# Optimization experiments

Hardware: AMD Instinct MI355X
Metric: run time of the kernel (lower is better)

Reference implementation:

```python
import math
import jax, jax.numpy as jnp
import numpy as np

N_HEADS = 8
FACTOR = 1


def setup_inputs() -> dict:
    key = jax.random.key(0)
    ks = jax.random.split(key, 8)
    B, L, D = 8, 2048, 512
    scale = 0.05
    return {
        "queries": jax.random.normal(ks[0], (B, L, D), jnp.float32),
        "keys": jax.random.normal(ks[1], (B, L, D), jnp.float32),
        "values": jax.random.normal(ks[2], (B, L, D), jnp.float32),
        "Wq": jax.random.normal(ks[3], (D, D), jnp.float32) * scale,
        "bq": jnp.zeros((D,), jnp.float32),
        "Wk": jax.random.normal(ks[4], (D, D), jnp.float32) * scale,
        "bk": jnp.zeros((D,), jnp.float32),
        "Wv": jax.random.normal(ks[5], (D, D), jnp.float32) * scale,
        "bv": jnp.zeros((D,), jnp.float32),
        "Wo": jax.random.normal(ks[6], (D, D), jnp.float32) * scale,
        "bo": jnp.zeros((D,), jnp.float32),
    }


def _autocorrelation(q, k, v):
    # q,k,v: [B, L, H, E]; L == S assumed (as built in setup_inputs)
    B, L, H, E = q.shape
    qp = jnp.transpose(q, (0, 2, 3, 1))  # [B,H,E,L]
    kp = jnp.transpose(k, (0, 2, 3, 1))
    vp = jnp.transpose(v, (0, 2, 3, 1))
    q_fft = jnp.fft.rfft(qp, axis=-1)
    k_fft = jnp.fft.rfft(kp, axis=-1)
    corr = jnp.fft.irfft(q_fft * jnp.conj(k_fft), n=L, axis=-1)  # [B,H,E,L]

    # training-path time-delay aggregation
    top_k = int(FACTOR * math.log(L))  # static python int
    mean_value = corr.mean(axis=(1, 2))  # [B, L]
    _, index = jax.lax.top_k(mean_value.mean(axis=0), top_k)  # [K] global delays
    weights = mean_value[:, index]  # [B, K]
    tmp_corr = jax.nn.softmax(weights, axis=-1)  # [B, K]
    # roll(v, -d) along last axis == gather at (t + d) mod L
    idx = (jnp.arange(L)[None, :] + index[:, None]) % L  # [K, L]
    patterns = vp[..., idx]  # [B,H,E,K,L]
    delays_agg = jnp.einsum('bhekl,bk->bhel', patterns, tmp_corr)  # [B,H,E,L]
    return jnp.transpose(delays_agg, (0, 3, 1, 2))  # [B,L,H,E]


def reference(queries, keys, values, Wq, bq, Wk, bk, Wv, bv, Wo, bo):
    B, L, Dm = queries.shape
    H = N_HEADS
    q = (queries @ Wq + bq).reshape(B, L, H, -1)
    k = (keys @ Wk + bk).reshape(B, L, H, -1)
    v = (values @ Wv + bv).reshape(B, L, H, -1)
    out = _autocorrelation(q, k, v).reshape(B, L, -1)
    return out @ Wo + bo
```

## Files before the change

kernel.cpp:

```cpp
#include <hip/hip_runtime.h>
#include <stdint.h>

#define BATCH 8
#define L_SEQ 2048
#define D_MODEL 512
#define TOPK 7
#define BM 128
#define BN 128
#define BK 32
#define LK 40
#define LT 136

typedef _Float16 f16x8 __attribute__((ext_vector_type(8)));
typedef __attribute__((ext_vector_type(4))) float f32x4;
typedef unsigned short u16;
typedef unsigned int u32;

__device__ __forceinline__ u16 f2h(float f) {
    union { _Float16 h; u16 u; } v; v.h = (_Float16)f; return v.u;
}

__device__ __forceinline__ void load_lds16(const u16* g, u16* l) {
    __builtin_amdgcn_global_load_lds(
        (const __attribute__((address_space(1))) u32*)(g),
        (__attribute__((address_space(3))) u32*)(l), 16, 0, 0);
}

__global__ __launch_bounds__(256) void gemm_qkv(
    const float* __restrict__ Xq, const float* __restrict__ Xk, const float* __restrict__ Xv,
    const u16* __restrict__ Wqt, const u16* __restrict__ Wkt, const u16* __restrict__ Wvt,
    const float* __restrict__ bq, const float* __restrict__ bk, const float* __restrict__ bv,
    u16* __restrict__ QT, u16* __restrict__ KT, u16* __restrict__ Vout)
{
    __shared__ __align__(16) u16 smem[BM * LK + BN * BK];
    u16* lA = smem;
    u16* lB = smem + BM * LK;
    u16* lT = smem;

    const int tid = threadIdx.x;
    const int hw = blockIdx.x;
    const int lg = (hw & 7) * 192 + (hw >> 3);
    const int bn = lg & 3, bm = (lg >> 2) & 127, z = lg >> 9;

    const int lane = tid & 63, wave = tid >> 6;
    const int wm = wave >> 1, wn = wave & 1;
    const int l15 = lane & 15, quad = lane >> 4;

    const float* A  = (z == 0) ? Xq  : (z == 1) ? Xk  : Xv;
    const u16*   Bt = (z == 0) ? Wqt : (z == 1) ? Wkt : Wvt;
    const float* bias = (z == 0) ? bq : (z == 1) ? bk : bv;

    const int s0 = wave * 64 + lane, s1 = s0 + 256;
    const int r0 = s0 >> 2, c0 = (s0 & 3) ^ ((r0 >> 1) & 3);
    const int r1 = s1 >> 2, c1 = (s1 & 3) ^ ((r1 >> 1) & 3);
    const u16* gB0 = Bt + (long)(bn * BN + r0) * D_MODEL + c0 * 8;
    const u16* gB1 = Bt + (long)(bn * BN + r1) * D_MODEL + c1 * 8;
    u16* lB0 = &lB[wave * 512]; u16* lB1 = &lB[2048 + wave * 512];

    f32x4 acc[4][4] = {};

    for (int k0 = 0; k0 < D_MODEL; k0 += BK) {
        load_lds16(gB0, lB0); load_lds16(gB1, lB1);
        gB0 += BK; gB1 += BK;
        #pragma unroll
        for (int j = 0; j < 4; ++j) {
            int idx = tid + j * 256;
            int row = idx >> 3, c4 = (idx & 7) * 4;
            float4 va = *(const float4*)(A + (long)(bm * BM + row) * D_MODEL + k0 + c4);
            ushort4 pa;
            pa.x = f2h(va.x); pa.y = f2h(va.y); pa.z = f2h(va.z); pa.w = f2h(va.w);
            *(ushort4*)&lA[row * LK + c4] = pa;
        }
        __syncthreads();

        f16x8 fa[4], fb[4];
        #pragma unroll
        for (int i = 0; i < 4; ++i)
            fa[i] = *(const f16x8*)&lA[(wm * 64 + i * 16 + l15) * LK + quad * 8];
        #pragma unroll
        for (int j = 0; j < 4; ++j) {
            int n = wn * 64 + j * 16 + l15;
            int cs = quad ^ ((n >> 1) & 3);
            fb[j] = *(const f16x8*)&lB[n * 32 + cs * 8];
        }
        #pragma unroll
        for (int i = 0; i < 4; ++i)
            #pragma unroll
            for (int j = 0; j < 4; ++j)
                acc[i][j] = __builtin_amdgcn_mfma_f32_16x16x32_f16(fa[i], fb[j], acc[i][j], 0, 0, 0);
        __syncthreads();
    }

    if (z < 2) {
        u16* out = (z == 0) ? QT : KT;
        const int t0 = (bm * BM) & (L_SEQ - 1);
        const int bb = (bm * BM) >> 11;
        #pragma unroll
        for (int h = 0; h < 2; ++h) {
            __syncthreads();
            if (wn == h) {
                #pragma unroll
                for (int j = 0; j < 4; ++j) {
                    int dloc = j * 16 + l15;
                    float bvv = bias[bn * BN + h * 64 + dloc];
                    #pragma unroll
                    for (int i = 0; i < 4; ++i) {
                        int trow = wm * 64 + i * 16 + quad * 4;
                        #pragma unroll
                        for (int r = 0; r < 4; ++r)
                            lT[dloc * LT + trow + r] = f2h(acc[i][j][r] + bvv);
                    }
                }
            }
            __syncthreads();
            int dloc = tid >> 2, q4 = tid & 3;
            long base = ((long)(bb * D_MODEL + bn * BN + h * 64 + dloc)) * L_SEQ + t0;
            #pragma unroll
            for (int s = 0; s < 4; ++s) {
                int c = q4 * 4 + s;
                *(uint4*)(out + base + c * 8) = *(const uint4*)&lT[dloc * LT + c * 8];
            }
        }
    } else {
        #pragma unroll
        for (int i = 0; i < 4; ++i) {
            int row = bm * BM + wm * 64 + i * 16 + quad * 4;
            #pragma unroll
            for (int j = 0; j < 4; ++j) {
                int col = bn * BN + wn * 64 + j * 16 + l15;
                float bvv = bias[col];
                #pragma unroll
                for (int r = 0; r < 4; ++r)
                    Vout[(long)(row + r) * D_MODEL + col] = f2h(acc[i][j][r] + bvv);
            }
        }
    }
}

__global__ __launch_bounds__(256) void gemm_out_fused(
    const u16* __restrict__ V, const u16* __restrict__ Bt,
    const int* __restrict__ selIdx, const float* __restrict__ selW,
    const float* __restrict__ bias, float* __restrict__ Cp)
{
    __shared__ __align__(16) u16 lA[BM * LK];
    __shared__ __align__(16) u16 lB[BN * BK];
    __shared__ int   si[TOPK];
    __shared__ float sw[BATCH][TOPK];

    const int tid = threadIdx.x;
    const int hw = blockIdx.x;
    const int lg = (hw & 7) * 64 + (hw >> 3);
    const int bn = lg & 3, bm = lg >> 2;

    const int lane = tid & 63, wave = tid >> 6;
    const int wm = wave >> 1, wn = wave & 1;
    const int l15 = lane & 15, quad = lane >> 4;

    if (tid < TOPK) si[tid] = selIdx[tid];
    if (tid < BATCH * TOPK) sw[tid / TOPK][tid % TOPK] = selW[tid];

    const int s0 = wave * 64 + lane, s1 = s0 + 256;
    const int r0 = s0 >> 2, c0 = (s0 & 3) ^ ((r0 >> 1) & 3);
    const int r1 = s1 >> 2, c1 = (s1 & 3) ^ ((r1 >> 1) & 3);
    const u16* gB0 = Bt + (long)(bn * BN + r0) * D_MODEL + c0 * 8;
    const u16* gB1 = Bt + (long)(bn * BN + r1) * D_MODEL + c1 * 8;
    u16* lB0 = &lB[wave * 512]; u16* lB1 = &lB[2048 + wave * 512];

    __syncthreads();

    f32x4 acc[4][4] = {};

    for (int k0 = 0; k0 < D_MODEL; k0 += BK) {
        load_lds16(gB0, lB0); load_lds16(gB1, lB1);
        gB0 += BK; gB1 += BK;
        #pragma unroll
        for (int j = 0; j < 2; ++j) {
            int idx = tid + j * 256;
            int row = idx >> 2, c8 = (idx & 3) * 8;
            int gr = bm * BM + row;
            int b = gr >> 11, l = gr & (L_SEQ - 1);
            float a[8] = {0,0,0,0,0,0,0,0};
            #pragma unroll
            for (int k = 0; k < TOPK; ++k) {
                int src = (l + si[k]) & (L_SEQ - 1);
                union { uint4 u; _Float16 h[8]; } x;
                x.u = *(const uint4*)(V + ((long)b * L_SEQ + src) * D_MODEL + k0 + c8);
                float w = sw[b][k];
                #pragma unroll
                for (int q = 0; q < 8; ++q) a[q] += w * (float)x.h[q];
            }
            union { uint4 u; u16 s[8]; } o;
            #pragma unroll
            for (int q = 0; q < 8; ++q) o.s[q] = f2h(a[q]);
            *(uint4*)&lA[row * LK + c8] = o.u;
        }
        __syncthreads();

        f16x8 fa[4], fb[4];
        #pragma unroll
        for (int i = 0; i < 4; ++i)
            fa[i] = *(const f16x8*)&lA[(wm * 64 + i * 16 + l15) * LK + quad * 8];
        #pragma unroll
        for (int j = 0; j < 4; ++j) {
            int n = wn * 64 + j * 16 + l15;
            int cs = quad ^ ((n >> 1) & 3);
            fb[j] = *(const f16x8*)&lB[n * 32 + cs * 8];
        }
        #pragma unroll
        for (int i = 0; i < 4; ++i)
            #pragma unroll
            for (int j = 0; j < 4; ++j)
                acc[i][j] = __builtin_amdgcn_mfma_f32_16x16x32_f16(fa[i], fb[j], acc[i][j], 0, 0, 0);
        __syncthreads();
    }

    #pragma unroll
    for (int i = 0; i < 4; ++i) {
        int row = bm * BM + wm * 64 + i * 16 + quad * 4;
        #pragma unroll
        for (int j = 0; j < 4; ++j) {
            int col = bn * BN + wn * 64 + j * 16 + l15;
            float bvv = bias[col];
            #pragma unroll
            for (int r = 0; r < 4; ++r)
                Cp[(long)(row + r) * D_MODEL + col] = acc[i][j][r] + bvv;
        }
    }
}

__device__ __forceinline__ void fft2048_lds(
    float* Zr, float* Zi, const float* Twr, const float* Twi, int tid)
{
    #pragma unroll
    for (int s = 0; s < 10; s += 2) {
        #pragma unroll
        for (int u = 0; u < 2; ++u) {
            int idx = tid + u * 256;
            int d1 = 1 << s;
            int pos = idx & (d1 - 1);
            int i0 = ((idx >> s) << (s + 2)) + pos;
            float w1r = Twr[pos << (10 - s)], w1i = Twi[pos << (10 - s)];
            float w2r = Twr[pos << (9 - s)],  w2i = Twi[pos << (9 - s)];
            int p2 = pos + d1;
            float w3r = Twr[p2 << (9 - s)],   w3i = Twi[p2 << (9 - s)];
            float ar = Zr[i0],          ai = Zi[i0];
            float br = Zr[i0 + d1],     bi = Zi[i0 + d1];
            float cr = Zr[i0 + 2 * d1], ci = Zi[i0 + 2 * d1];
            float dr = Zr[i0 + 3 * d1], di = Zi[i0 + 3 * d1];
            float t1r = br * w1r - bi * w1i, t1i = br * w1i + bi * w1r;
            float Ar = ar + t1r, Ai = ai + t1i, Br = ar - t1r, Bi = ai - t1i;
            float t2r = dr * w1r - di * w1i, t2i = dr * w1i + di * w1r;
            float Cr = cr + t2r, Ci = ci + t2i, Dr = cr - t2r, Di = ci - t2i;
            float u1r = Cr * w2r - Ci * w2i, u1i = Cr * w2i + Ci * w2r;
            float u2r = Dr * w3r - Di * w3i, u2i = Dr * w3i + Di * w3r;
            Zr[i0]          = Ar + u1r; Zi[i0]          = Ai + u1i;
            Zr[i0 + 2 * d1] = Ar - u1r; Zi[i0 + 2 * d1] = Ai - u1i;
            Zr[i0 + d1]     = Br + u2r; Zi[i0 + d1]     = Bi + u2i;
            Zr[i0 + 3 * d1] = Br - u2r; Zi[i0 + 3 * d1] = Bi - u2i;
        }
        __syncthreads();
    }
    #pragma unroll
    for (int j = 0; j < 4; ++j) {
        int idx = tid + j * 256;
        float wr = Twr[idx], wi = Twi[idx];
        float ar = Zr[idx], ai = Zi[idx];
        float br = Zr[idx + 1024], bi = Zi[idx + 1024];
        float tr = br * wr - bi * wi, ti = br * wi + bi * wr;
        Zr[idx] = ar + tr; Zi[idx] = ai + ti;
        Zr[idx + 1024] = ar - tr; Zi[idx + 1024] = ai - ti;
    }
    __syncthreads();
}

__global__ __launch_bounds__(256) void fft_corr_fwd(
    const u16* __restrict__ QT, const u16* __restrict__ KT, float* __restrict__ S)
{
    __shared__ float Zr[2048], Zi[2048];
    __shared__ float Sr[2048], Si[2048];
    __shared__ float Twr[1024], Twi[1024];
    const int tid = threadIdx.x;
    const int b = blockIdx.x >> 6, dg = blockIdx.x & 63;

    #pragma unroll
    for (int j = 0; j < 4; ++j) {
        int i = tid + j * 256;
        float ang = -6.28318530717958647692f * (float)i * (1.0f / 2048.0f);
        float sn, cs; __sincosf(ang, &sn, &cs);
        Twr[i] = cs; Twi[i] = sn;
    }
    #pragma unroll
    for (int j = 0; j < 8; ++j) { Sr[tid + j * 256] = 0.f; Si[tid + j * 256] = 0.f; }

    for (int g = 0; g < 8; ++g) {
        int d = dg * 8 + g;
        const u16* qrow = QT + ((long)b * D_MODEL + d) * L_SEQ;
        const u16* krow = KT + ((long)b * D_MODEL + d) * L_SEQ;
        __syncthreads();
        union { uint4 u; _Float16 h[8]; } xq, xk;
        xq.u = *(const uint4*)(qrow + tid * 8);
        xk.u = *(const uint4*)(krow + tid * 8);
        #pragma unroll
        for (int j = 0; j < 8; ++j) {
            int t = tid * 8 + j;
            int tr = (int)(__brev((unsigned)t) >> 21);
            Zr[tr] = (float)xq.h[j];
            Zi[tr] = (float)xk.h[j];
        }
        __syncthreads();
        fft2048_lds(Zr, Zi, Twr, Twi, tid);
        #pragma unroll
        for (int j = 0; j < 8; ++j) {
            int f = tid + j * 256;
            int fm = (2048 - f) & 2047;
            float Xr = Zr[f], Xi = Zi[f], Xmr = Zr[fm], Xmi = Zi[fm];
            float qr = 0.5f * (Xr + Xmr), qi = 0.5f * (Xi - Xmi);
            float dr = Xr - Xmr,          di = Xi + Xmi;
            float kr = 0.5f * di,         ki = -0.5f * dr;
            Sr[f] += qr * kr + qi * ki;
            Si[f] += qi * kr - qr * ki;
        }
    }
    __syncthreads();
    #pragma unroll
    for (int j = 0; j < 8; ++j) {
        int f = tid + j * 256;
        atomicAdd(&S[((long)b * 2048 + f) * 2 + 0], Sr[f]);
        atomicAdd(&S[((long)b * 2048 + f) * 2 + 1], Si[f]);
    }
}

__global__ __launch_bounds__(256) void fft_corr_inv(
    const float* __restrict__ S, float* __restrict__ raw)
{
    __shared__ float Zr[2048], Zi[2048];
    __shared__ float Twr[1024], Twi[1024];
    const int tid = threadIdx.x;
    const int b = blockIdx.x;

    #pragma unroll
    for (int j = 0; j < 4; ++j) {
        int i = tid + j * 256;
        float ang = 6.28318530717958647692f * (float)i * (1.0f / 2048.0f);
        float sn, cs; __sincosf(ang, &sn, &cs);
        Twr[i] = cs; Twi[i] = sn;
    }
    #pragma unroll
    for (int j = 0; j < 8; ++j) {
        int f = tid + j * 256;
        int fr = (int)(__brev((unsigned)f) >> 21);
        Zr[fr] = S[((long)b * 2048 + f) * 2 + 0];
        Zi[fr] = S[((long)b * 2048 + f) * 2 + 1];
    }
    __syncthreads();
    fft2048_lds(Zr, Zi, Twr, Twi, tid);
    #pragma unroll
    for (int j = 0; j < 8; ++j) {
        int t = tid + j * 256;
        raw[(long)b * 2048 + t] = Zr[t] * (1.0f / 2048.0f);
    }
}

__global__ __launch_bounds__(256) void transposeW4(
    const float* __restrict__ Wq, const float* __restrict__ Wk,
    const float* __restrict__ Wv, const float* __restrict__ Wo, u16* __restrict__ dstBase)
{
    __shared__ float t[32][33];
    const int z = blockIdx.z;
    const float* src = (z == 0) ? Wq : (z == 1) ? Wk : (z == 2) ? Wv : Wo;
    u16* dst = dstBase + (long)z * D_MODEL * D_MODEL;
    int tx = threadIdx.x & 31, ty = threadIdx.x >> 5;
    int c0 = blockIdx.x * 32, r0 = blockIdx.y * 32;
    #pragma unroll
    for (int r = ty; r < 32; r += 8)
        t[r][tx] = src[(long)(r0 + r) * D_MODEL + c0 + tx];
    __syncthreads();
    #pragma unroll
    for (int r = ty; r < 32; r += 8)
        dst[(long)(c0 + r) * D_MODEL + r0 + tx] = f2h(t[tx][r]);
}

__global__ __launch_bounds__(256) void select_topk(
    const float* __restrict__ raw, int* __restrict__ selIdx, float* __restrict__ selW)
{
    __shared__ float g[L_SEQ];
    __shared__ float rv[256];
    __shared__ int   ri[256];
    __shared__ int   sidx[TOPK];
    __shared__ float wbuf[BATCH][TOPK];
    int tid = threadIdx.x;
    for (int t = tid; t < L_SEQ; t += 256) {
        float s = 0.0f;
        #pragma unroll
        for (int b = 0; b < BATCH; ++b) s += raw[b * L_SEQ + t];
        g[t] = s;
    }
    __syncthreads();
    for (int it = 0; it < TOPK; ++it) {
        float best = -1e30f; int bi = 0x7fffffff;
        for (int t = tid; t < L_SEQ; t += 256) {
            float v = g[t];
            if (v > best || (v == best && t < bi)) { best = v; bi = t; }
        }
        rv[tid] = best; ri[tid] = bi;
        __syncthreads();
        for (int s = 128; s > 0; s >>= 1) {
            if (tid < s) {
                float v2 = rv[tid + s]; int i2 = ri[tid + s];
                if (v2 > rv[tid] || (v2 == rv[tid] && i2 < ri[tid])) { rv[tid] = v2; ri[tid] = i2; }
            }
            __syncthreads();
        }
        if (tid == 0) { sidx[it] = ri[0]; g[ri[0]] = -1e30f; }
        __syncthreads();
    }
    if (tid < BATCH * TOPK) {
        int b = tid / TOPK, k = tid % TOPK;
        wbuf[b][k] = raw[b * L_SEQ + sidx[k]] * (1.0f / 512.0f);
    }
    __syncthreads();
    if (tid < BATCH) {
        float mx = -1e30f;
        #pragma unroll
        for (int k = 0; k < TOPK; ++k) mx = fmaxf(mx, wbuf[tid][k]);
        float e[TOPK]; float sum = 0.0f;
        #pragma unroll
        for (int k = 0; k < TOPK; ++k) { e[k] = expf(wbuf[tid][k] - mx); sum += e[k]; }
        #pragma unroll
        for (int k = 0; k < TOPK; ++k) selW[tid * TOPK + k] = e[k] / sum;
    }
    if (tid < TOPK) selIdx[tid] = sidx[tid];
}

extern "C" void kernel_launch(void* const* d_in, const int* in_sizes, int n_in,
                              void* d_out, int out_size, void* d_ws, size_t ws_size,
                              hipStream_t stream)
{
    (void)in_sizes; (void)n_in; (void)out_size; (void)ws_size;
    const float* Xq = (const float*)d_in[0];
    const float* Xk = (const float*)d_in[1];
    const float* Xv = (const float*)d_in[2];
    const float* Wq = (const float*)d_in[3];
    const float* bq = (const float*)d_in[4];
    const float* Wk = (const float*)d_in[5];
    const float* bk = (const float*)d_in[6];
    const float* Wv = (const float*)d_in[7];
    const float* bv = (const float*)d_in[8];
    const float* Wo = (const float*)d_in[9];
    const float* bo = (const float*)d_in[10];

    char* ws = (char*)d_ws;
    const long SLABH = (long)BATCH * L_SEQ * D_MODEL * sizeof(u16);
    u16* QT   = (u16*)(ws);
    u16* KT   = (u16*)(ws + SLABH);
    u16* Vf   = (u16*)(ws + 2 * SLABH);
    const long WSZ = (long)D_MODEL * D_MODEL;
    u16* Wt   = (u16*)(ws + 3 * SLABH);
    u16* Wqt = Wt + 0 * WSZ; u16* Wkt = Wt + 1 * WSZ;
    u16* Wvt = Wt + 2 * WSZ; u16* Wot = Wt + 3 * WSZ;
    float* S   = (float*)(ws + 3 * SLABH + 4 * WSZ * sizeof(u16));
    float* raw = S + (long)BATCH * L_SEQ * 2;
    int*   sIdx = (int*)(raw + (long)BATCH * L_SEQ);
    float* sW   = (float*)(sIdx + 8);

    dim3 tb(256);
    transposeW4<<<dim3(16, 16, 4), tb, 0, stream>>>(Wq, Wk, Wv, Wo, Wt);
    hipMemsetAsync(S, 0, (long)BATCH * L_SEQ * 2 * sizeof(float), stream);

    gemm_qkv<<<dim3(1536), tb, 0, stream>>>(Xq, Xk, Xv, Wqt, Wkt, Wvt, bq, bk, bv, QT, KT, Vf);

    fft_corr_fwd<<<dim3(512), tb, 0, stream>>>(QT, KT, S);
    fft_corr_inv<<<dim3(BATCH), tb, 0, stream>>>(S, raw);
    select_topk<<<1, tb, 0, stream>>>(raw, sIdx, sW);

    gemm_out_fused<<<dim3(512), tb, 0, stream>>>(Vf, Wot, sIdx, sW, bo, (float*)d_out);
}
```

Measured before the change: 333.7 us.

## Double-buffer LDS in QKV and output GEMMs, use wave shuffles in top-k

```diff
diff --git a/kernel.cpp b/kernel.cpp
--- a/kernel.cpp
+++ b/kernel.cpp
@@ -26,16 +26,15 @@
         (__attribute__((address_space(3))) u32*)(l), 16, 0, 0);
 }
 
-__global__ __launch_bounds__(256) void gemm_qkv(
+__global__ __launch_bounds__(256, 3) void gemm_qkv(
     const float* __restrict__ Xq, const float* __restrict__ Xk, const float* __restrict__ Xv,
     const u16* __restrict__ Wqt, const u16* __restrict__ Wkt, const u16* __restrict__ Wvt,
     const float* __restrict__ bq, const float* __restrict__ bk, const float* __restrict__ bv,
     u16* __restrict__ QT, u16* __restrict__ KT, u16* __restrict__ Vout)
 {
-    __shared__ __align__(16) u16 smem[BM * LK + BN * BK];
-    u16* lA = smem;
-    u16* lB = smem + BM * LK;
+    __shared__ __align__(16) u16 smem[2 * BM * LK + 2 * BN * BK];
     u16* lT = smem;
+    u16* lBb = smem + 2 * BM * LK;
 
     const int tid = threadIdx.x;
     const int hw = blockIdx.x;
@@ -55,39 +54,74 @@
     const int r1 = s1 >> 2, c1 = (s1 & 3) ^ ((r1 >> 1) & 3);
     const u16* gB0 = Bt + (long)(bn * BN + r0) * D_MODEL + c0 * 8;
     const u16* gB1 = Bt + (long)(bn * BN + r1) * D_MODEL + c1 * 8;
-    u16* lB0 = &lB[wave * 512]; u16* lB1 = &lB[2048 + wave * 512];
 
     f32x4 acc[4][4] = {};
 
-    for (int k0 = 0; k0 < D_MODEL; k0 += BK) {
-        load_lds16(gB0, lB0); load_lds16(gB1, lB1);
+    {
+        load_lds16(gB0, lBb + wave * 512);
+        load_lds16(gB1, lBb + 2048 + wave * 512);
         gB0 += BK; gB1 += BK;
         #pragma unroll
         for (int j = 0; j < 4; ++j) {
             int idx = tid + j * 256;
             int row = idx >> 3, c4 = (idx & 7) * 4;
-            float4 va = *(const float4*)(A + (long)(bm * BM + row) * D_MODEL + k0 + c4);
+            float4 va = *(const float4*)(A + (long)(bm * BM + row) * D_MODEL + c4);
             ushort4 pa;
             pa.x = f2h(va.x); pa.y = f2h(va.y); pa.z = f2h(va.z); pa.w = f2h(va.w);
-            *(ushort4*)&lA[row * LK + c4] = pa;
-        }
-        __syncthreads();
+            *(ushort4*)&smem[row * LK + c4] = pa;
+        }
+    }
+    __syncthreads();
+
+    for (int t = 0; t < 16; ++t) {
+        const int cur = t & 1;
+        u16* lAc = smem + cur * (BM * LK);
+        u16* lBc = lBb + cur * (BN * BK);
+        u16* lAn = smem + (cur ^ 1) * (BM * LK);
+        u16* lBn = lBb + (cur ^ 1) * (BN * BK);
+        const bool nx = (t < 15);
+        const int k1 = (t + 1) * BK;
+
+        float4 va[4];
+        if (nx) {
+            load_lds16(gB0, lBn + wave * 512);
+            load_lds16(gB1, lBn + 2048 + wave * 512);
+            gB0 += BK; gB1 += BK;
+            #pragma unroll
+            for (int j = 0; j < 4; ++j) {
+                int idx = tid + j * 256;
+                int row = idx >> 3, c4 = (idx & 7) * 4;
+                va[j] = *(const float4*)(A + (long)(bm * BM + row) * D_MODEL + k1 + c4);
+            }
+        }
 
         f16x8 fa[4], fb[4];
         #pragma unroll
         for (int i = 0; i < 4; ++i)
-            fa[i] = *(const f16x8*)&lA[(wm * 64 + i * 16 + l15) * LK + quad * 8];
+            fa[i] = *(const f16x8*)&lAc[(wm * 64 + i * 16 + l15) * LK + quad * 8];
         #pragma unroll
         for (int j = 0; j < 4; ++j) {
             int n = wn * 64 + j * 16 + l15;
             int cs = quad ^ ((n >> 1) & 3);
-            fb[j] = *(const f16x8*)&lB[n * 32 + cs * 8];
+            fb[j] = *(const f16x8*)&lBc[n * 32 + cs * 8];
         }
         #pragma unroll
         for (int i = 0; i < 4; ++i)
             #pragma unroll
             for (int j = 0; j < 4; ++j)
                 acc[i][j] = __builtin_amdgcn_mfma_f32_16x16x32_f16(fa[i], fb[j], acc[i][j], 0, 0, 0);
+
+        if (nx) {
+            #pragma unroll
+            for (int j = 0; j < 4; ++j) {
+                int idx = tid + j * 256;
+                int row = idx >> 3, c4 = (idx & 7) * 4;
+                ushort4 pa;
+                pa.x = f2h(va[j].x); pa.y = f2h(va[j].y);
+                pa.z = f2h(va[j].z); pa.w = f2h(va[j].w);
+                *(ushort4*)&lAn[row * LK + c4] = pa;
+            }
+        }
         __syncthreads();
     }
 
@@ -137,13 +171,13 @@
     }
 }
 
-__global__ __launch_bounds__(256) void gemm_out_fused(
+__global__ __launch_bounds__(256, 3) void gemm_out_fused(
     const u16* __restrict__ V, const u16* __restrict__ Bt,
     const int* __restrict__ selIdx, const float* __restrict__ selW,
     const float* __restrict__ bias, float* __restrict__ Cp)
 {
-    __shared__ __align__(16) u16 lA[BM * LK];
-    __shared__ __align__(16) u16 lB[BN * BK];
+    __shared__ __align__(16) u16 lA[2 * BM * LK];
+    __shared__ __align__(16) u16 lB[2 * BN * BK];
     __shared__ int   si[TOPK];
     __shared__ float sw[BATCH][TOPK];
 
@@ -164,27 +198,32 @@
     const int r1 = s1 >> 2, c1 = (s1 & 3) ^ ((r1 >> 1) & 3);
     const u16* gB0 = Bt + (long)(bn * BN + r0) * D_MODEL + c0 * 8;
     const u16* gB1 = Bt + (long)(bn * BN + r1) * D_MODEL + c1 * 8;
-    u16* lB0 = &lB[wave * 512]; u16* lB1 = &lB[2048 + wave * 512];
-
-    __syncthreads();
+
+    const int row_a = tid >> 2,          c8_a = (tid & 3) * 8;
+    const int row_b = (tid + 256) >> 2,  c8_b = (tid & 3) * 8;
+    const int gra = bm * BM + row_a, grb = bm * BM + row_b;
+    const int ba = gra >> 11, la = gra & (L_SEQ - 1);
+    const int bb = grb >> 11, lb = grb & (L_SEQ - 1);
+
+    __syncthreads();
+
+    union U8 { uint4 u; _Float16 h[8]; };
 
     f32x4 acc[4][4] = {};
 
-    for (int k0 = 0; k0 < D_MODEL; k0 += BK) {
-        load_lds16(gB0, lB0); load_lds16(gB1, lB1);
+    {
+        load_lds16(gB0, lB + wave * 512);
+        load_lds16(gB1, lB + 2048 + wave * 512);
         gB0 += BK; gB1 += BK;
         #pragma unroll
         for (int j = 0; j < 2; ++j) {
-            int idx = tid + j * 256;
-            int row = idx >> 2, c8 = (idx & 3) * 8;
-            int gr = bm * BM + row;
-            int b = gr >> 11, l = gr & (L_SEQ - 1);
+            int row = j ? row_b : row_a, c8 = j ? c8_b : c8_a;
+            int b = j ? bb : ba, l = j ? lb : la;
             float a[8] = {0,0,0,0,0,0,0,0};
             #pragma unroll
             for (int k = 0; k < TOPK; ++k) {
                 int src = (l + si[k]) & (L_SEQ - 1);
-                union { uint4 u; _Float16 h[8]; } x;
-                x.u = *(const uint4*)(V + ((long)b * L_SEQ + src) * D_MODEL + k0 + c8);
+                U8 x; x.u = *(const uint4*)(V + ((long)b * L_SEQ + src) * D_MODEL + c8);
                 float w = sw[b][k];
                 #pragma unroll
                 for (int q = 0; q < 8; ++q) a[q] += w * (float)x.h[q];
@@ -194,23 +233,86 @@
             for (int q = 0; q < 8; ++q) o.s[q] = f2h(a[q]);
             *(uint4*)&lA[row * LK + c8] = o.u;
         }
-        __syncthreads();
+    }
+    __syncthreads();
+
+    for (int t = 0; t < 16; ++t) {
+        const int cur = t & 1;
+        u16* lAc = lA + cur * (BM * LK);
+        u16* lBc = lB + cur * (BN * BK);
+        u16* lAn = lA + (cur ^ 1) * (BM * LK);
+        u16* lBn = lB + (cur ^ 1) * (BN * BK);
+        const bool nx = (t < 15);
+        const int k1 = (t + 1) * BK;
+
+        U8 xv[7];
+        if (nx) {
+            load_lds16(gB0, lBn + wave * 512);
+            load_lds16(gB1, lBn + 2048 + wave * 512);
+            gB0 += BK; gB1 += BK;
+            #pragma unroll
+            for (int k = 0; k < TOPK; ++k) {
+                int src = (la + si[k]) & (L_SEQ - 1);
+                xv[k].u = *(const uint4*)(V + ((long)ba * L_SEQ + src) * D_MODEL + k1 + c8_a);
+            }
+        }
 
         f16x8 fa[4], fb[4];
         #pragma unroll
         for (int i = 0; i < 4; ++i)
-            fa[i] = *(const f16x8*)&lA[(wm * 64 + i * 16 + l15) * LK + quad * 8];
+            fa[i] = *(const f16x8*)&lAc[(wm * 64 + i * 16 + l15) * LK + quad * 8];
         #pragma unroll
         for (int j = 0; j < 4; ++j) {
             int n = wn * 64 + j * 16 + l15;
             int cs = quad ^ ((n >> 1) & 3);
-            fb[j] = *(const f16x8*)&lB[n * 32 + cs * 8];
-        }
-        #pragma unroll
-        for (int i = 0; i < 4; ++i)
+            fb[j] = *(const f16x8*)&lBc[n * 32 + cs * 8];
+        }
+
+        #pragma unroll
+        for (int i = 0; i < 2; ++i)
             #pragma unroll
             for (int j = 0; j < 4; ++j)
                 acc[i][j] = __builtin_amdgcn_mfma_f32_16x16x32_f16(fa[i], fb[j], acc[i][j], 0, 0, 0);
+
+        U8 xw[7];
+        if (nx) {
+            float a[8] = {0,0,0,0,0,0,0,0};
+            #pragma unroll
+            for (int k = 0; k < TOPK; ++k) {
+                float w = sw[ba][k];
+                #pragma unroll
+                for (int q = 0; q < 8; ++q) a[q] += w * (float)xv[k].h[q];
+            }
+            union { uint4 u; u16 s[8]; } o;
+            #pragma unroll
+            for (int q = 0; q < 8; ++q) o.s[q] = f2h(a[q]);
+            *(uint4*)&lAn[row_a * LK + c8_a] = o.u;
+            #pragma unroll
+            for (int k = 0; k < TOPK; ++k) {
+                int src = (lb + si[k]) & (L_SEQ - 1);
+                xw[k].u = *(const uint4*)(V + ((long)bb * L_SEQ + src) * D_MODEL + k1 + c8_b);
+            }
+        }
+
+        #pragma unroll
+        for (int i = 2; i < 4; ++i)
+            #pragma unroll
+            for (int j = 0; j < 4; ++j)
+                acc[i][j] = __builtin_amdgcn_mfma_f32_16x16x32_f16(fa[i], fb[j], acc[i][j], 0, 0, 0);
+
+        if (nx) {
+            float a[8] = {0,0,0,0,0,0,0,0};
+            #pragma unroll
+            for (int k = 0; k < TOPK; ++k) {
+                float w = sw[bb][k];
+                #pragma unroll
+                for (int q = 0; q < 8; ++q) a[q] += w * (float)xw[k].h[q];
+            }
+            union { uint4 u; u16 s[8]; } o;
+            #pragma unroll
+            for (int q = 0; q < 8; ++q) o.s[q] = f2h(a[q]);
+            *(uint4*)&lAn[row_b * LK + c8_b] = o.u;
+        }
         __syncthreads();
     }
 
@@ -384,11 +486,12 @@
     const float* __restrict__ raw, int* __restrict__ selIdx, float* __restrict__ selW)
 {
     __shared__ float g[L_SEQ];
-    __shared__ float rv[256];
-    __shared__ int   ri[256];
+    __shared__ float wv[4];
+    __shared__ int   wi[4];
     __shared__ int   sidx[TOPK];
     __shared__ float wbuf[BATCH][TOPK];
     int tid = threadIdx.x;
+    int lane = tid & 63, wave = tid >> 6;
     for (int t = tid; t < L_SEQ; t += 256) {
         float s = 0.0f;
         #pragma unroll
@@ -398,20 +501,27 @@
     __syncthreads();
     for (int it = 0; it < TOPK; ++it) {
         float best = -1e30f; int bi = 0x7fffffff;
-        for (int t = tid; t < L_SEQ; t += 256) {
+        #pragma unroll
+        for (int j = 0; j < 8; ++j) {
+            int t = tid + j * 256;
             float v = g[t];
             if (v > best || (v == best && t < bi)) { best = v; bi = t; }
         }
-        rv[tid] = best; ri[tid] = bi;
-        __syncthreads();
-        for (int s = 128; s > 0; s >>= 1) {
-            if (tid < s) {
-                float v2 = rv[tid + s]; int i2 = ri[tid + s];
-                if (v2 > rv[tid] || (v2 == rv[tid] && i2 < ri[tid])) { rv[tid] = v2; ri[tid] = i2; }
-            }
-            __syncthreads();
-        }
-        if (tid == 0) { sidx[it] = ri[0]; g[ri[0]] = -1e30f; }
+        #pragma unroll
+        for (int s = 32; s > 0; s >>= 1) {
+            float v2 = __shfl_xor(best, s);
+            int   i2 = __shfl_xor(bi, s);
+            if (v2 > best || (v2 == best && i2 < bi)) { best = v2; bi = i2; }
+        }
+        if (lane == 0) { wv[wave] = best; wi[wave] = bi; }
+        __syncthreads();
+        if (tid == 0) {
+            float b0 = wv[0]; int i0 = wi[0];
+            #pragma unroll
+            for (int w = 1; w < 4; ++w)
+                if (wv[w] > b0 || (wv[w] == b0 && wi[w] < i0)) { b0 = wv[w]; i0 = wi[w]; }
+            sidx[it] = i0; g[i0] = -1e30f;
+        }
         __syncthreads();
     }
     if (tid < BATCH * TOPK) {
```

New measurement: 317.8 us. -4.8%, faster.
